# Performance work log

Measured on AMD Instinct MI355X. Metric: run time of the kernel, lower is better.

Reference implementation:

```python
import jax, jax.numpy as jnp
import numpy as np

REFN, RN, G = 4, 2, 1          # reference views, query-group repeat, n_groups
NH, DH = 4, 32                 # heads, head channels
C = NH * DH                    # 128
H = W = 64
STRIDE, KS = 2, 3
HK, WK = H // STRIDE, W // STRIDE
L = 2048                       # query tokens per batch element
OFR = 2.0                      # offset_range_factor
SCALE = DH ** -0.5


def _grid_sample(img, grid):
    # img: (N, Ch, H, W); grid: (N, Hg, Wg, 2) xy in [-1,1]
    # bilinear, align_corners=True, padding_mode='zeros' (matches F.grid_sample)
    N, Ch, Hh, Ww = img.shape
    gx = (grid[..., 0] + 1.0) * 0.5 * (Ww - 1)
    gy = (grid[..., 1] + 1.0) * 0.5 * (Hh - 1)
    x0 = jnp.floor(gx); y0 = jnp.floor(gy)
    x1, y1 = x0 + 1.0, y0 + 1.0

    def gather(xi, yi):
        valid = ((xi >= 0) & (xi <= Ww - 1) & (yi >= 0) & (yi <= Hh - 1))
        xc = jnp.clip(xi, 0, Ww - 1).astype(jnp.int32)
        yc = jnp.clip(yi, 0, Hh - 1).astype(jnp.int32)
        g = jax.vmap(lambda im, yy, xx: im[:, yy, xx])(img, yc, xc)  # (N,Ch,Hg,Wg)
        return g * valid[:, None].astype(img.dtype)

    wa = (x1 - gx) * (y1 - gy); wb = (gx - x0) * (y1 - gy)
    wc = (x1 - gx) * (gy - y0); wd = (gx - x0) * (gy - y0)
    return (gather(x0, y0) * wa[:, None] + gather(x1, y0) * wb[:, None]
            + gather(x0, y1) * wc[:, None] + gather(x1, y1) * wd[:, None])


def setup_inputs():
    key = jax.random.key(0)
    ks = jax.random.split(key, 10)
    s = 0.05  # keep logits in a sane range with random weights
    return {
        "x": jax.random.normal(ks[0], (REFN, C, H, W), jnp.float32),
        "y": jax.random.normal(ks[1], (REFN, C, H, W), jnp.float32),
        "q_": jax.random.normal(ks[2], (RN * REFN, L, C), jnp.float32),
        "mask_": jnp.ones((RN * REFN, L, 1), jnp.float32),
        "Wq": jax.random.normal(ks[3], (C, C), jnp.float32) * s,
        "bq": jnp.zeros((C,), jnp.float32),
        "Wmd": jax.random.normal(ks[4], (C, C), jnp.float32) * s,
        "dw_w": jax.random.normal(ks[5], (C, 1, KS, KS), jnp.float32) * s,
        "dw_b": jnp.zeros((C,), jnp.float32),
        "ln_g": jnp.ones((C,), jnp.float32),
        "ln_b": jnp.zeros((C,), jnp.float32),
        "off_w": jax.random.normal(ks[6], (2, C), jnp.float32) * s,
        "Wk": jax.random.normal(ks[7], (C, C), jnp.float32) * s,
        "bk": jnp.zeros((C,), jnp.float32),
        "Wv": jax.random.normal(ks[8], (C, C), jnp.float32) * s,
        "bv": jnp.zeros((C,), jnp.float32),
        "Wo": jax.random.normal(ks[9], (C, C), jnp.float32) * s,
        "bo": jnp.zeros((C,), jnp.float32),
    }


def _forward(x, y, q_, mask_, Wq, bq, Wmd, dw_w, dw_b, ln_g, ln_b, off_w,
             Wk, bk, Wv, bv, Wo, bo):
    B = q_.shape[0]
    # masked mean over tokens -> modulation vector, then proj_q (Linear)
    q_cond = jnp.sum(q_ * mask_, 1) / (jnp.sum(mask_, 1) + 1e-6)   # (B, C)
    q_cond = q_cond @ Wq.T + bq

    xb = jnp.tile(x, (RN, 1, 1, 1))                                 # (B, C, H, W)

    # Conv2DMod (StyleGAN2 modulated 1x1 conv, demod eps 1e-8)
    wmod = Wmd[None] * (q_cond[:, None, :] + 1.0)                   # (B, Cout, Cin)
    wmod = wmod * jax.lax.rsqrt(jnp.sum(wmod * wmod, -1, keepdims=True) + 1e-8)
    q_t = jnp.einsum('boi,bihw->bohw', wmod, xb)                    # (B, C, H, W)

    # conv_offset: depthwise 3x3 s2 -> LayerNorm(channel) -> GELU -> 1x1 (no bias)
    t = jax.lax.conv_general_dilated(
        q_t, dw_w, (STRIDE, STRIDE), ((1, 1), (1, 1)),
        feature_group_count=C, dimension_numbers=('NCHW', 'OIHW', 'NCHW'))
    t = t + dw_b[None, :, None, None]
    mu = jnp.mean(t, 1, keepdims=True)
    var = jnp.mean((t - mu) ** 2, 1, keepdims=True)
    t = (t - mu) * jax.lax.rsqrt(var + 1e-5)
    t = t * ln_g[None, :, None, None] + ln_b[None, :, None, None]
    t = jax.nn.gelu(t, approximate=False)
    offset = jnp.einsum('oc,bchw->bohw', off_w, t)                  # (B*G, 2, HK, WK)

    orange = jnp.array([1.0 / (HK - 1), 1.0 / (WK - 1)], jnp.float32).reshape(1, 2, 1, 1)
    offset = jnp.tanh(offset) * orange * OFR
    offset = jnp.transpose(offset, (0, 2, 3, 1))                    # (B*G, HK, WK, 2) yx

    ry = (jnp.linspace(0.5, HK - 0.5, HK) / (HK - 1.0)) * 2.0 - 1.0
    rx = (jnp.linspace(0.5, WK - 0.5, WK) / (WK - 1.0)) * 2.0 - 1.0
    ref = jnp.stack(jnp.meshgrid(ry, rx, indexing='ij'), -1)        # (HK, WK, 2) yx
    ref = jnp.broadcast_to(ref[None], (B * G, HK, WK, 2))

    pos = offset + ref            # offset_range_factor >= 0 -> no clamp
    pos = pos[..., ::-1]          # yx -> xy for grid_sample
    ns = HK * WK
    # '(rn refn gn) h w n -> (refn gn) rn (h w) n'  (G == 1)
    grid = pos.reshape(RN, REFN, ns, 2).transpose(1, 0, 2, 3)       # (REFN, RN, ns, 2)

    xs = _grid_sample(y, grid)                                      # (REFN, C, RN, ns)
    # 'refn c (rn gn) (h w) -> (rn refn gn) c h w'  (G == 1)
    xs = xs.transpose(2, 0, 1, 3).reshape(B, C, ns)                 # (B, C, ns)

    k = (jnp.einsum('oc,bcn->bon', Wk, xs) + bk[None, :, None]).reshape(B * NH, DH, ns)
    v = (jnp.einsum('oc,bcn->bon', Wv, xs) + bv[None, :, None]).reshape(B * NH, DH, ns)
    q = jnp.transpose(q_, (0, 2, 1)).reshape(B * NH, DH, -1)        # (B*NH, DH, L)

    attn = jnp.einsum('bcm,bcn->bmn', q, k) * SCALE                 # (B*NH, L, ns)
    # NOTE: original calls attn.masked_fill(...) WITHOUT assignment (non in-place)
    # so the mask has no effect on attention -- faithfully omitted.
    attn = jax.nn.softmax(attn, axis=-1)
    out = jnp.einsum('bmn,bcn->bcm', attn, v)                       # (B*NH, DH, L)
    out = out.reshape(B, C, -1).transpose(0, 2, 1)                  # (B, L, C), G == 1
    yo = out @ Wo.T + bo
    return yo, grid.reshape(B, G, HK, WK, 2), ref.reshape(B, G, HK, WK, 2)


def reference(x, y, q_, mask_, Wq, bq, Wmd, dw_w, dw_b, ln_g, ln_b, off_w,
              Wk, bk, Wv, bv, Wo, bo):
    return _forward(x, y, q_, mask_, Wq, bq, Wmd, dw_w, dw_b, ln_g, ln_b, off_w,
                    Wk, bk, Wv, bv, Wo, bo)
```

## Files before the change

### kernel.cpp

```cpp
#include <hip/hip_runtime.h>
#include <math.h>


#define SCALE_F 0.17677669529663687f

typedef __attribute__((ext_vector_type(8))) short short8v;
typedef __attribute__((ext_vector_type(8))) unsigned short u16x8;
typedef __attribute__((ext_vector_type(4))) unsigned short u16x4;
typedef __attribute__((ext_vector_type(4))) float f32x4;

static __device__ __forceinline__ unsigned short f2bf(float f) {
  unsigned int u = __builtin_bit_cast(unsigned int, f);
  u += 0x7fffu + ((u >> 16) & 1u);
  return (unsigned short)(u >> 16);
}

__global__ void kt_wb(const float* __restrict__ Wk, const float* __restrict__ Wv,
                      const float* __restrict__ Wo, unsigned short* __restrict__ Wkb,
                      unsigned short* __restrict__ Wvb, unsigned short* __restrict__ Wob) {
  int idx = blockIdx.x * 256 + threadIdx.x;
  Wkb[idx] = f2bf(Wk[idx]);
  Wvb[idx] = f2bf(Wv[idx]);
  Wob[idx] = f2bf(Wo[idx]);
}

__global__ void kt_transpose_y(const float* __restrict__ y, float* __restrict__ y_t) {
  __shared__ __align__(16) float tile[128][65];
  int bid = blockIdx.x;
  int n = bid >> 6, yy = bid & 63;
  int t = threadIdx.x;
  for (int p = 0; p < 32; ++p) {
    int idx = p * 256 + t;
    int c = idx >> 6, xx = idx & 63;
    tile[c][xx] = y[((n * 128 + c) * 64 + yy) * 64 + xx];
  }
  __syncthreads();
  for (int p = 0; p < 32; ++p) {
    int idx = p * 256 + t;
    int xx = idx >> 7, c = idx & 127;
    y_t[((n * 64 + yy) * 64 + xx) * 128 + c] = tile[c][xx];
  }
}

__global__ void kt_xT(const float* __restrict__ x, unsigned short* __restrict__ xTb) {
  __shared__ float tile[128][65];
  int bid = blockIdx.x;
  int n = bid >> 6, yy = bid & 63;
  int t = threadIdx.x;
  for (int p = 0; p < 32; ++p) {
    int idx = p * 256 + t;
    int c = idx >> 6, xx = idx & 63;
    tile[c][xx] = x[((n * 128 + c) * 64 + yy) * 64 + xx];
  }
  __syncthreads();
  for (int p = 0; p < 4; ++p) {
    int idx = p * 256 + t;
    int xx = idx >> 4, g = idx & 15;
    u16x8 v;
#pragma unroll
    for (int j = 0; j < 8; ++j) v[j] = f2bf(tile[g * 8 + j][xx]);
    *reinterpret_cast<u16x8*>(
        xTb + ((size_t)n * 4096 + yy * 64 + xx) * 128 + g * 8) = v;
  }
}

__global__ void k_qsum(const float* __restrict__ q_, const float* __restrict__ mask_,
                       float* __restrict__ qpart, float* __restrict__ mpart) {
  int b = blockIdx.x, ch = blockIdx.y, c = threadIdx.x;
  float acc = 0.f, ma = 0.f;
  for (int mm = 0; mm < 64; ++mm) {
    int m = ch * 64 + mm;
    float mk = mask_[b * 2048 + m];
    acc += q_[(b * 2048 + m) * 128 + c] * mk;
    ma += mk;
  }
  qpart[(b * 32 + ch) * 128 + c] = acc;
  if (c == 0) mpart[b * 32 + ch] = ma;
}

__global__ void k_wmod(const float* __restrict__ qpart, const float* __restrict__ mpart,
                       const float* __restrict__ Wq, const float* __restrict__ bq,
                       const float* __restrict__ Wmd, unsigned short* __restrict__ wmodb) {
  int b = blockIdx.x, c = threadIdx.x;
  __shared__ float qc[128], q2[128];
  float s = 0.f, ms = 0.f;
  for (int ch = 0; ch < 32; ++ch) {
    s += qpart[(b * 32 + ch) * 128 + c];
    ms += mpart[b * 32 + ch];
  }
  qc[c] = s / (ms + 1e-6f);
  __syncthreads();
  float acc = bq[c];
  for (int i = 0; i < 128; ++i) acc += qc[i] * Wq[c * 128 + i];
  q2[c] = acc + 1.0f;
  __syncthreads();
  float nrm = 0.f;
  for (int i = 0; i < 128; ++i) {
    float wv = Wmd[c * 128 + i] * q2[i];
    nrm += wv * wv;
  }
  float rs = 1.0f / sqrtf(nrm + 1e-8f);
  for (int i = 0; i < 128; ++i)
    wmodb[(b * 128 + c) * 128 + i] = f2bf(Wmd[c * 128 + i] * q2[i] * rs);
}

__global__ __launch_bounds__(256) void k_qt_mfma(
    const unsigned short* __restrict__ wmodb,
    const unsigned short* __restrict__ xTb,
    float* __restrict__ q_t) {
  int b = blockIdx.x;
  int n0 = blockIdx.y * 128;
  int t = threadIdx.x;
  int w = t >> 6, l = t & 63;
  int lr = l & 15, lg = l >> 4;

  __shared__ __align__(16) unsigned short Asw[128 * 128];
  __shared__ __align__(16) unsigned short Bsw[128 * 128];
  char* Ab = reinterpret_cast<char*>(Asw);
  char* Bb = reinterpret_cast<char*>(Bsw);

  const unsigned short* asrc = wmodb + (size_t)b * 128 * 128;
  const unsigned short* bsrc = xTb + ((size_t)(b & 3) * 4096 + n0) * 128;
#pragma unroll
  for (int it = 0; it < 8; ++it) {
    int idx = it * 256 + t;
    int row = idx >> 4, cb = (idx & 15) * 16;
    int dst = row * 256 + (cb ^ ((row & 7) << 4));
    *reinterpret_cast<u16x8*>(Ab + dst) = *reinterpret_cast<const u16x8*>(asrc + idx * 8);
    *reinterpret_cast<u16x8*>(Bb + dst) = *reinterpret_cast<const u16x8*>(bsrc + idx * 8);
  }
  __syncthreads();

  const f32x4 z4 = {0.f, 0.f, 0.f, 0.f};
  f32x4 acc[8][2];
#pragma unroll
  for (int mf = 0; mf < 8; ++mf) { acc[mf][0] = z4; acc[mf][1] = z4; }

#pragma unroll
  for (int ks = 0; ks < 4; ++ks) {
    int cb = ks * 64 + lg * 16;
    short8v bf[2];
#pragma unroll
    for (int nf = 0; nf < 2; ++nf) {
      int row = w * 32 + nf * 16 + lr;
      bf[nf] = *reinterpret_cast<const short8v*>(Bb + row * 256 + (cb ^ ((row & 7) << 4)));
    }
#pragma unroll
    for (int mf = 0; mf < 8; ++mf) {
      int row = mf * 16 + lr;
      short8v af = *reinterpret_cast<const short8v*>(Ab + row * 256 + (cb ^ ((row & 7) << 4)));
      acc[mf][0] = __builtin_amdgcn_mfma_f32_16x16x32_bf16(af, bf[0], acc[mf][0], 0, 0, 0);
      acc[mf][1] = __builtin_amdgcn_mfma_f32_16x16x32_bf16(af, bf[1], acc[mf][1], 0, 0, 0);
    }
  }

#pragma unroll
  for (int mf = 0; mf < 8; ++mf)
#pragma unroll
    for (int nf = 0; nf < 2; ++nf)
#pragma unroll
      for (int r = 0; r < 4; ++r) {
        int o = mf * 16 + lg * 4 + r;
        int px = n0 + w * 32 + nf * 16 + lr;
        q_t[((size_t)(b * 128 + o)) * 4096 + px] = acc[mf][nf][r];
      }
}

__global__ void k_dwconv(const float* __restrict__ q_t, const float* __restrict__ dw_w,
                         const float* __restrict__ dw_b, float* __restrict__ t0) {
  int bid = blockIdx.x;
  int t = threadIdx.x;
  int b = bid >> 9;
  int c = (bid >> 2) & 127;
  int px = (bid & 3) * 256 + t;
  int i = px >> 5, j = px & 31;
  float w[9];
#pragma unroll
  for (int q = 0; q < 9; ++q) w[q] = dw_w[c * 9 + q];
  const float* src = q_t + (b * 128 + c) * 4096;
  float acc = dw_b[c];
#pragma unroll
  for (int dy = 0; dy < 3; ++dy) {
    int yy = 2 * i - 1 + dy;
    if (yy < 0 || yy > 63) continue;
#pragma unroll
    for (int dx = 0; dx < 3; ++dx) {
      int xx = 2 * j - 1 + dx;
      if (xx < 0 || xx > 63) continue;
      acc += w[dy * 3 + dx] * src[yy * 64 + xx];
    }
  }
  t0[(b * 128 + c) * 1024 + px] = acc;
}

__global__ void k_ln_off(const float* __restrict__ t0, const float* __restrict__ ln_g,
                         const float* __restrict__ ln_b, const float* __restrict__ off_w,
                         float* __restrict__ posg, float* __restrict__ grid_out,
                         float* __restrict__ ref_out) {
  int b = blockIdx.x;
  int s = blockIdx.y * 64 + threadIdx.x;
  int i = s >> 5, j = s & 31;
  const float* src = t0 + b * 128 * 1024 + s;
  float sum = 0.f, sq = 0.f;
  for (int c = 0; c < 128; ++c) {
    float v = src[c * 1024];
    sum += v; sq += v * v;
  }
  float mu = sum * (1.0f / 128.0f);
  float var = sq * (1.0f / 128.0f) - mu * mu;
  float rstd = 1.0f / sqrtf(var + 1e-5f);
  float off0 = 0.f, off1 = 0.f;
  for (int c = 0; c < 128; ++c) {
    float v = src[c * 1024];
    float xn = (v - mu) * rstd * ln_g[c] + ln_b[c];
    float g = 0.5f * xn * (1.0f + erff(xn * 0.7071067811865476f));
    off0 += off_w[c] * g;
    off1 += off_w[128 + c] * g;
  }
  float offy = tanhf(off0) * (1.0f / 31.0f) * 2.0f;
  float offx = tanhf(off1) * (1.0f / 31.0f) * 2.0f;
  float ry = (0.5f + (float)i) / 31.0f * 2.0f - 1.0f;
  float rx = (0.5f + (float)j) / 31.0f * 2.0f - 1.0f;
  float posy = offy + ry;
  float posx = offx + rx;
  int bp = (b & 3) * 2 + (b >> 2);
  float2 g2; g2.x = posx; g2.y = posy;
  *reinterpret_cast<float2*>(&grid_out[(bp * 1024 + s) * 2]) = g2;
  float2 r2; r2.x = ry; r2.y = rx;
  *reinterpret_cast<float2*>(&ref_out[(b * 1024 + s) * 2]) = r2;
  float2 p2;
  p2.x = (posx + 1.0f) * 0.5f * 63.0f;
  p2.y = (posy + 1.0f) * 0.5f * 63.0f;
  *reinterpret_cast<float2*>(&posg[(b * 1024 + s) * 2]) = p2;
}

__global__ void k_gsample(const float* __restrict__ y_t, const float* __restrict__ posg,
                          unsigned short* __restrict__ xsb) {
  int b = blockIdx.x;
  int s = blockIdx.y * 2 + (threadIdx.x >> 7);
  int c = threadIdx.x & 127;
  float gx = posg[(b * 1024 + s) * 2 + 0];
  float gy = posg[(b * 1024 + s) * 2 + 1];
  float x0 = floorf(gx), y0 = floorf(gy);
  float x1 = x0 + 1.0f, y1 = y0 + 1.0f;
  float wa = (x1 - gx) * (y1 - gy);
  float wb = (gx - x0) * (y1 - gy);
  float wc = (x1 - gx) * (gy - y0);
  float wd = (gx - x0) * (gy - y0);
  int n = b & 3;
  const float* base = y_t + n * 64 * 64 * 128 + c;
  float acc = 0.f;
  if (x0 >= 0.f && x0 <= 63.f && y0 >= 0.f && y0 <= 63.f)
    acc += wa * base[((int)y0 * 64 + (int)x0) * 128];
  if (x1 >= 0.f && x1 <= 63.f && y0 >= 0.f && y0 <= 63.f)
    acc += wb * base[((int)y0 * 64 + (int)x1) * 128];
  if (x0 >= 0.f && x0 <= 63.f && y1 >= 0.f && y1 <= 63.f)
    acc += wc * base[((int)y1 * 64 + (int)x0) * 128];
  if (x1 >= 0.f && x1 <= 63.f && y1 >= 0.f && y1 <= 63.f)
    acc += wd * base[((int)y1 * 64 + (int)x1) * 128];
  xsb[(b * 1024 + s) * 128 + c] = f2bf(acc);
}

__global__ __launch_bounds__(256) void k_projkv_mfma(
    const unsigned short* __restrict__ xsb, const unsigned short* __restrict__ Wkb,
    const unsigned short* __restrict__ Wvb, const float* __restrict__ bk,
    const float* __restrict__ bv, unsigned short* __restrict__ kb,
    unsigned short* __restrict__ vb) {
  int b = blockIdx.x, nt = blockIdx.y, z = blockIdx.z;
  int t = threadIdx.x;
  int w = t >> 6, l = t & 63;
  int lr = l & 15, lg = l >> 4;

  __shared__ __align__(16) unsigned short Asw[128 * 128];
  __shared__ __align__(16) unsigned short Bsw[128 * 128];
  char* Ab = reinterpret_cast<char*>(Asw);
  char* Bb = reinterpret_cast<char*>(Bsw);

  const unsigned short* asrc = (z == 0) ? Wkb : Wvb;
  const unsigned short* bsrc = xsb + ((size_t)b * 1024 + nt * 128) * 128;
  const float* bias = (z == 0) ? bk : bv;
#pragma unroll
  for (int it = 0; it < 8; ++it) {
    int idx = it * 256 + t;
    int row = idx >> 4, cb = (idx & 15) * 16;
    int dst = row * 256 + (cb ^ ((row & 7) << 4));
    *reinterpret_cast<u16x8*>(Ab + dst) = *reinterpret_cast<const u16x8*>(asrc + idx * 8);
    *reinterpret_cast<u16x8*>(Bb + dst) = *reinterpret_cast<const u16x8*>(bsrc + idx * 8);
  }
  __syncthreads();

  const f32x4 z4 = {0.f, 0.f, 0.f, 0.f};
  f32x4 acc[8][2];
#pragma unroll
  for (int mf = 0; mf < 8; ++mf) { acc[mf][0] = z4; acc[mf][1] = z4; }

#pragma unroll
  for (int ks = 0; ks < 4; ++ks) {
    int cb = ks * 64 + lg * 16;
    short8v bf[2];
#pragma unroll
    for (int nf = 0; nf < 2; ++nf) {
      int row = w * 32 + nf * 16 + lr;
      bf[nf] = *reinterpret_cast<const short8v*>(Bb + row * 256 + (cb ^ ((row & 7) << 4)));
    }
#pragma unroll
    for (int mf = 0; mf < 8; ++mf) {
      int row = mf * 16 + lr;
      short8v af = *reinterpret_cast<const short8v*>(Ab + row * 256 + (cb ^ ((row & 7) << 4)));
      acc[mf][0] = __builtin_amdgcn_mfma_f32_16x16x32_bf16(af, bf[0], acc[mf][0], 0, 0, 0);
      acc[mf][1] = __builtin_amdgcn_mfma_f32_16x16x32_bf16(af, bf[1], acc[mf][1], 0, 0, 0);
    }
  }

  if (z == 0) {
#pragma unroll
    for (int mf = 0; mf < 8; ++mf) {
      int o0 = mf * 16 + lg * 4;
      int h = o0 >> 5, d0 = o0 & 31;
#pragma unroll
      for (int nf = 0; nf < 2; ++nf) {
        int n = nt * 128 + w * 32 + nf * 16 + lr;
        u16x4 pk;
#pragma unroll
        for (int r = 0; r < 4; ++r) pk[r] = f2bf(acc[mf][nf][r] + bias[o0 + r]);
        *reinterpret_cast<u16x4*>(kb + ((size_t)(b * 4 + h) * 1024 + n) * 32 + d0) = pk;
      }
    }
  } else {
#pragma unroll
    for (int mf = 0; mf < 8; ++mf)
#pragma unroll
      for (int nf = 0; nf < 2; ++nf)
#pragma unroll
        for (int r = 0; r < 4; ++r) {
          int o = mf * 16 + lg * 4 + r;
          int n = nt * 128 + w * 32 + nf * 16 + lr;
          vb[(size_t)(b * 128 + o) * 1024 + n] = f2bf(acc[mf][nf][r] + bias[o]);
        }
  }
}

__global__ __launch_bounds__(256) void k_attn_mfma(
    const float* __restrict__ q_, const unsigned short* __restrict__ kb,
    const unsigned short* __restrict__ vb, unsigned short* __restrict__ obmcb) {
  int bh = blockIdx.x;
  int b = bh >> 2, h = bh & 3;
  int m0 = blockIdx.y * 128;
  int t = threadIdx.x;
  int w = t >> 6, l = t & 63;
  int lr = l & 15, lg = l >> 4;

  __shared__ __align__(16) unsigned short K_lds[4 * 64 * 8];
  __shared__ __align__(16) unsigned short V_lds[8 * 32 * 8];
  __shared__ __align__(16) unsigned short P_lds[4 * 256 * 8];

  short8v qa[2];
#pragma unroll
  for (int mf = 0; mf < 2; ++mf) {
    int m = m0 + w * 32 + mf * 16 + lr;
    const float* qp = q_ + ((size_t)(b * 2048 + m)) * 128 + h * 32 + lg * 8;
    float4 x0 = *reinterpret_cast<const float4*>(qp);
    float4 x1 = *reinterpret_cast<const float4*>(qp + 4);
    float vals[8] = {x0.x, x0.y, x0.z, x0.w, x1.x, x1.y, x1.z, x1.w};
    short8v q8;
#pragma unroll
    for (int j = 0; j < 8; ++j) q8[j] = (short)f2bf(vals[j] * SCALE_F);
    qa[mf] = q8;
  }

  const f32x4 z4 = {0.f, 0.f, 0.f, 0.f};
  f32x4 oacc[2][2];
  float lsum[2][4];
#pragma unroll
  for (int mf = 0; mf < 2; ++mf) {
#pragma unroll
    for (int df = 0; df < 2; ++df) oacc[mf][df] = z4;
#pragma unroll
    for (int r = 0; r < 4; ++r) lsum[mf][r] = 0.f;
  }

  const unsigned short* kbase = kb + (size_t)bh * 1024 * 32;
  const unsigned short* vbase = vb + (size_t)bh * 32 * 1024;

  for (int nt = 0; nt < 16; ++nt) {
    __syncthreads();
    {
      int dblk = t >> 6, n = t & 63;
      u16x8 kv = *reinterpret_cast<const u16x8*>(kbase + ((size_t)(nt * 64 + n)) * 32 + dblk * 8);
      *reinterpret_cast<u16x8*>(&K_lds[t * 8]) = kv;
    }
    {
      int nblk = t >> 5, d = t & 31;
      u16x8 vv = *reinterpret_cast<const u16x8*>(vbase + (size_t)d * 1024 + nt * 64 + nblk * 8);
      *reinterpret_cast<u16x8*>(&V_lds[t * 8]) = vv;
    }
    __syncthreads();

    short8v kfr[4];
#pragma unroll
    for (int nf = 0; nf < 4; ++nf)
      kfr[nf] = *reinterpret_cast<const short8v*>(&K_lds[(lg * 64 + nf * 16 + lr) * 8]);
    f32x4 s[2][4];
#pragma unroll
    for (int mf = 0; mf < 2; ++mf)
#pragma unroll
      for (int nf = 0; nf < 4; ++nf)
        s[mf][nf] = __builtin_amdgcn_mfma_f32_16x16x32_bf16(qa[mf], kfr[nf], z4, 0, 0, 0);

#pragma unroll
    for (int mf = 0; mf < 2; ++mf) {
#pragma unroll
      for (int nf = 0; nf < 4; ++nf) {
        int sbase = (w * 256 + (nf * 2 + (lr >> 3)) * 32 + mf * 16 + lg * 4) * 8 + (lr & 7);
#pragma unroll
        for (int r = 0; r < 4; ++r) {
          float pe = __expf(s[mf][nf][r]);
          lsum[mf][r] += pe;
          P_lds[sbase + r * 8] = f2bf(pe);
        }
      }
    }
    __syncthreads();

#pragma unroll
    for (int ks = 0; ks < 2; ++ks) {
      short8v pa[2], vf[2];
#pragma unroll
      for (int mf = 0; mf < 2; ++mf)
        pa[mf] = *reinterpret_cast<const short8v*>(
            &P_lds[(w * 256 + (ks * 4 + lg) * 32 + mf * 16 + lr) * 8]);
#pragma unroll
      for (int df = 0; df < 2; ++df)
        vf[df] = *reinterpret_cast<const short8v*>(
            &V_lds[((ks * 4 + lg) * 32 + df * 16 + lr) * 8]);
#pragma unroll
      for (int mf = 0; mf < 2; ++mf)
#pragma unroll
        for (int df = 0; df < 2; ++df)
          oacc[mf][df] = __builtin_amdgcn_mfma_f32_16x16x32_bf16(pa[mf], vf[df], oacc[mf][df], 0, 0, 0);
    }
  }

#pragma unroll
  for (int mf = 0; mf < 2; ++mf) {
#pragma unroll
    for (int r = 0; r < 4; ++r) {
      float v = lsum[mf][r];
      v += __shfl_xor(v, 1); v += __shfl_xor(v, 2);
      v += __shfl_xor(v, 4); v += __shfl_xor(v, 8);
      float inv = 1.0f / v;
      int m = m0 + w * 32 + mf * 16 + lg * 4 + r;
      unsigned short* op = obmcb + ((size_t)(b * 2048 + m)) * 128 + h * 32;
      op[lr] = f2bf(oacc[mf][0][r] * inv);
      op[16 + lr] = f2bf(oacc[mf][1][r] * inv);
    }
  }
}

__global__ __launch_bounds__(256) void k_out_mfma(
    const unsigned short* __restrict__ obmcb, const unsigned short* __restrict__ Wob,
    const float* __restrict__ bo, float* __restrict__ yo) {
  int b = blockIdx.x, mt = blockIdx.y;
  int t = threadIdx.x;
  int w = t >> 6, l = t & 63;
  int lr = l & 15, lg = l >> 4;

  __shared__ __align__(16) unsigned short Asw[128 * 128];
  __shared__ __align__(16) unsigned short Bsw[128 * 128];
  char* Ab = reinterpret_cast<char*>(Asw);
  char* Bb = reinterpret_cast<char*>(Bsw);

  const unsigned short* bsrc = obmcb + ((size_t)b * 2048 + mt * 128) * 128;
#pragma unroll
  for (int it = 0; it < 8; ++it) {
    int idx = it * 256 + t;
    int row = idx >> 4, cb = (idx & 15) * 16;
    int dst = row * 256 + (cb ^ ((row & 7) << 4));
    *reinterpret_cast<u16x8*>(Ab + dst) = *reinterpret_cast<const u16x8*>(Wob + idx * 8);
    *reinterpret_cast<u16x8*>(Bb + dst) = *reinterpret_cast<const u16x8*>(bsrc + idx * 8);
  }
  __syncthreads();

  const f32x4 z4 = {0.f, 0.f, 0.f, 0.f};
  f32x4 acc[8][2];
#pragma unroll
  for (int mf = 0; mf < 8; ++mf) { acc[mf][0] = z4; acc[mf][1] = z4; }

#pragma unroll
  for (int ks = 0; ks < 4; ++ks) {
    int cb = ks * 64 + lg * 16;
    short8v bf[2];
#pragma unroll
    for (int nf = 0; nf < 2; ++nf) {
      int row = w * 32 + nf * 16 + lr;
      bf[nf] = *reinterpret_cast<const short8v*>(Bb + row * 256 + (cb ^ ((row & 7) << 4)));
    }
#pragma unroll
    for (int mf = 0; mf < 8; ++mf) {
      int row = mf * 16 + lr;
      short8v af = *reinterpret_cast<const short8v*>(Ab + row * 256 + (cb ^ ((row & 7) << 4)));
      acc[mf][0] = __builtin_amdgcn_mfma_f32_16x16x32_bf16(af, bf[0], acc[mf][0], 0, 0, 0);
      acc[mf][1] = __builtin_amdgcn_mfma_f32_16x16x32_bf16(af, bf[1], acc[mf][1], 0, 0, 0);
    }
  }

#pragma unroll
  for (int mf = 0; mf < 8; ++mf) {
    int o0 = mf * 16 + lg * 4;
#pragma unroll
    for (int nf = 0; nf < 2; ++nf) {
      int m = mt * 128 + w * 32 + nf * 16 + lr;
      float4 rv;
      rv.x = acc[mf][nf][0] + bo[o0 + 0];
      rv.y = acc[mf][nf][1] + bo[o0 + 1];
      rv.z = acc[mf][nf][2] + bo[o0 + 2];
      rv.w = acc[mf][nf][3] + bo[o0 + 3];
      *reinterpret_cast<float4*>(&yo[((size_t)(b * 2048 + m)) * 128 + o0]) = rv;
    }
  }
}

extern "C" void kernel_launch(void* const* d_in, const int* in_sizes, int n_in,
                              void* d_out, int out_size, void* d_ws, size_t ws_size,
                              hipStream_t stream) {
  const float* x     = (const float*)d_in[0];
  const float* y     = (const float*)d_in[1];
  const float* q_    = (const float*)d_in[2];
  const float* mask_ = (const float*)d_in[3];
  const float* Wq    = (const float*)d_in[4];
  const float* bq    = (const float*)d_in[5];
  const float* Wmd   = (const float*)d_in[6];
  const float* dw_w  = (const float*)d_in[7];
  const float* dw_b  = (const float*)d_in[8];
  const float* ln_g  = (const float*)d_in[9];
  const float* ln_b  = (const float*)d_in[10];
  const float* off_w = (const float*)d_in[11];
  const float* Wk    = (const float*)d_in[12];
  const float* bk    = (const float*)d_in[13];
  const float* Wv    = (const float*)d_in[14];
  const float* bv    = (const float*)d_in[15];
  const float* Wo    = (const float*)d_in[16];
  const float* bo    = (const float*)d_in[17];

  float* out = (float*)d_out;
  float* yo       = out;
  float* grid_out = out + 2097152;
  float* ref_out  = grid_out + 16384;

  float* ws    = (float*)d_ws;
  float* y_t   = ws;
  float* qpart = y_t + 2097152;
  float* mpart = qpart + 32768;
  float* q_t   = mpart + 256;
  float* t0    = q_t + 4194304;
  float* posg  = t0 + 1048576;
  unsigned short* kbb   = (unsigned short*)(posg + 16384);
  unsigned short* vbb   = kbb + 1048576;
  unsigned short* xTb   = vbb + 1048576;
  unsigned short* wmodb = xTb + 2097152;
  unsigned short* xsb   = wmodb + 131072;
  unsigned short* obmcb = xsb + 1048576;
  unsigned short* Wkb   = obmcb + 2097152;
  unsigned short* Wvb   = Wkb + 16384;
  unsigned short* Wob   = Wvb + 16384;

  hipLaunchKernelGGL(kt_wb, dim3(64), dim3(256), 0, stream, Wk, Wv, Wo, Wkb, Wvb, Wob);
  hipLaunchKernelGGL(kt_transpose_y, dim3(256), dim3(256), 0, stream, y, y_t);
  hipLaunchKernelGGL(kt_xT, dim3(256), dim3(256), 0, stream, x, xTb);
  hipLaunchKernelGGL(k_qsum, dim3(8, 32), dim3(128), 0, stream, q_, mask_, qpart, mpart);
  hipLaunchKernelGGL(k_wmod, dim3(8), dim3(128), 0, stream,
                     qpart, mpart, Wq, bq, Wmd, wmodb);
  hipLaunchKernelGGL(k_qt_mfma, dim3(8, 32), dim3(256), 0, stream, wmodb, xTb, q_t);
  hipLaunchKernelGGL(k_dwconv, dim3(4096), dim3(256), 0, stream, q_t, dw_w, dw_b, t0);
  hipLaunchKernelGGL(k_ln_off, dim3(8, 16), dim3(64), 0, stream,
                     t0, ln_g, ln_b, off_w, posg, grid_out, ref_out);
  hipLaunchKernelGGL(k_gsample, dim3(8, 512), dim3(256), 0, stream, y_t, posg, xsb);
  hipLaunchKernelGGL(k_projkv_mfma, dim3(8, 8, 2), dim3(256), 0, stream,
                     xsb, Wkb, Wvb, bk, bv, kbb, vbb);
  hipLaunchKernelGGL(k_attn_mfma, dim3(32, 16), dim3(256), 0, stream, q_, kbb, vbb, obmcb);
  hipLaunchKernelGGL(k_out_mfma, dim3(8, 16), dim3(256), 0, stream, obmcb, Wob, bo, yo);
}
```

Before: 215.8 us.

## Merge pack kernels, bf16 q_t, parallel LN reduce, double-buffer attention K/V

Merges the y and x transpose kernels into one launch and drops the weight-conversion kernel by converting Wk/Wv/Wo to bf16 while loading tiles in the consuming GEMMs. Stores the modulated query map in bf16 to halve the traffic into the depthwise conv. Gives the LayerNorm/offset kernel 256 threads with a shared tile and cross-group reduction. Double-buffers K/V in the attention loop with register prefetch, and swizzles the P tile to cut bank conflicts and barriers. The bf16 intermediate adds rounding error to the offsets and sampling positions.

```diff
diff --git a/kernel.cpp b/kernel.cpp
--- a/kernel.cpp
+++ b/kernel.cpp
@@ -14,53 +14,47 @@
   u += 0x7fffu + ((u >> 16) & 1u);
   return (unsigned short)(u >> 16);
 }
-
-__global__ void kt_wb(const float* __restrict__ Wk, const float* __restrict__ Wv,
-                      const float* __restrict__ Wo, unsigned short* __restrict__ Wkb,
-                      unsigned short* __restrict__ Wvb, unsigned short* __restrict__ Wob) {
-  int idx = blockIdx.x * 256 + threadIdx.x;
-  Wkb[idx] = f2bf(Wk[idx]);
-  Wvb[idx] = f2bf(Wv[idx]);
-  Wob[idx] = f2bf(Wo[idx]);
-}
-
-__global__ void kt_transpose_y(const float* __restrict__ y, float* __restrict__ y_t) {
+static __device__ __forceinline__ float bf2f(unsigned short s) {
+  unsigned int u = ((unsigned int)s) << 16;
+  return __builtin_bit_cast(float, u);
+}
+
+__global__ void kt_pack(const float* __restrict__ y, const float* __restrict__ x,
+                        float* __restrict__ y_t, unsigned short* __restrict__ xTb) {
   __shared__ __align__(16) float tile[128][65];
   int bid = blockIdx.x;
-  int n = bid >> 6, yy = bid & 63;
   int t = threadIdx.x;
-  for (int p = 0; p < 32; ++p) {
-    int idx = p * 256 + t;
-    int c = idx >> 6, xx = idx & 63;
-    tile[c][xx] = y[((n * 128 + c) * 64 + yy) * 64 + xx];
-  }
-  __syncthreads();
-  for (int p = 0; p < 32; ++p) {
-    int idx = p * 256 + t;
-    int xx = idx >> 7, c = idx & 127;
-    y_t[((n * 64 + yy) * 64 + xx) * 128 + c] = tile[c][xx];
-  }
-}
-
-__global__ void kt_xT(const float* __restrict__ x, unsigned short* __restrict__ xTb) {
-  __shared__ float tile[128][65];
-  int bid = blockIdx.x;
-  int n = bid >> 6, yy = bid & 63;
-  int t = threadIdx.x;
-  for (int p = 0; p < 32; ++p) {
-    int idx = p * 256 + t;
-    int c = idx >> 6, xx = idx & 63;
-    tile[c][xx] = x[((n * 128 + c) * 64 + yy) * 64 + xx];
-  }
-  __syncthreads();
-  for (int p = 0; p < 4; ++p) {
-    int idx = p * 256 + t;
-    int xx = idx >> 4, g = idx & 15;
-    u16x8 v;
-#pragma unroll
-    for (int j = 0; j < 8; ++j) v[j] = f2bf(tile[g * 8 + j][xx]);
-    *reinterpret_cast<u16x8*>(
-        xTb + ((size_t)n * 4096 + yy * 64 + xx) * 128 + g * 8) = v;
+  if (bid < 256) {
+    int n = bid >> 6, yy = bid & 63;
+    for (int p = 0; p < 32; ++p) {
+      int idx = p * 256 + t;
+      int c = idx >> 6, xx = idx & 63;
+      tile[c][xx] = y[((n * 128 + c) * 64 + yy) * 64 + xx];
+    }
+    __syncthreads();
+    for (int p = 0; p < 32; ++p) {
+      int idx = p * 256 + t;
+      int xx = idx >> 7, c = idx & 127;
+      y_t[((n * 64 + yy) * 64 + xx) * 128 + c] = tile[c][xx];
+    }
+  } else {
+    int nb = bid - 256;
+    int n = nb >> 6, yy = nb & 63;
+    for (int p = 0; p < 32; ++p) {
+      int idx = p * 256 + t;
+      int c = idx >> 6, xx = idx & 63;
+      tile[c][xx] = x[((n * 128 + c) * 64 + yy) * 64 + xx];
+    }
+    __syncthreads();
+    for (int p = 0; p < 4; ++p) {
+      int idx = p * 256 + t;
+      int xx = idx >> 4, g = idx & 15;
+      u16x8 v;
+#pragma unroll
+      for (int j = 0; j < 8; ++j) v[j] = f2bf(tile[g * 8 + j][xx]);
+      *reinterpret_cast<u16x8*>(
+          xTb + ((size_t)n * 4096 + yy * 64 + xx) * 128 + g * 8) = v;
+    }
   }
 }
 
@@ -107,7 +101,7 @@
 __global__ __launch_bounds__(256) void k_qt_mfma(
     const unsigned short* __restrict__ wmodb,
     const unsigned short* __restrict__ xTb,
-    float* __restrict__ q_t) {
+    unsigned short* __restrict__ q_tb) {
   int b = blockIdx.x;
   int n0 = blockIdx.y * 128;
   int t = threadIdx.x;
@@ -162,11 +156,12 @@
       for (int r = 0; r < 4; ++r) {
         int o = mf * 16 + lg * 4 + r;
         int px = n0 + w * 32 + nf * 16 + lr;
-        q_t[((size_t)(b * 128 + o)) * 4096 + px] = acc[mf][nf][r];
+        q_tb[((size_t)(b * 128 + o)) * 4096 + px] = f2bf(acc[mf][nf][r]);
       }
 }
 
-__global__ void k_dwconv(const float* __restrict__ q_t, const float* __restrict__ dw_w,
+__global__ void k_dwconv(const unsigned short* __restrict__ q_tb,
+                         const float* __restrict__ dw_w,
                          const float* __restrict__ dw_b, float* __restrict__ t0) {
   int bid = blockIdx.x;
   int t = threadIdx.x;
@@ -177,7 +172,7 @@
   float w[9];
 #pragma unroll
   for (int q = 0; q < 9; ++q) w[q] = dw_w[c * 9 + q];
-  const float* src = q_t + (b * 128 + c) * 4096;
+  const unsigned short* src = q_tb + (size_t)(b * 128 + c) * 4096;
   float acc = dw_b[c];
 #pragma unroll
   for (int dy = 0; dy < 3; ++dy) {
@@ -187,51 +182,76 @@
     for (int dx = 0; dx < 3; ++dx) {
       int xx = 2 * j - 1 + dx;
       if (xx < 0 || xx > 63) continue;
-      acc += w[dy * 3 + dx] * src[yy * 64 + xx];
+      acc += w[dy * 3 + dx] * bf2f(src[yy * 64 + xx]);
     }
   }
   t0[(b * 128 + c) * 1024 + px] = acc;
 }
 
-__global__ void k_ln_off(const float* __restrict__ t0, const float* __restrict__ ln_g,
-                         const float* __restrict__ ln_b, const float* __restrict__ off_w,
-                         float* __restrict__ posg, float* __restrict__ grid_out,
-                         float* __restrict__ ref_out) {
+__global__ __launch_bounds__(256) void k_ln_off(
+    const float* __restrict__ t0, const float* __restrict__ ln_g,
+    const float* __restrict__ ln_b, const float* __restrict__ off_w,
+    float* __restrict__ posg, float* __restrict__ grid_out,
+    float* __restrict__ ref_out) {
   int b = blockIdx.x;
-  int s = blockIdx.y * 64 + threadIdx.x;
-  int i = s >> 5, j = s & 31;
-  const float* src = t0 + b * 128 * 1024 + s;
+  int s0 = blockIdx.y * 64;
+  int t = threadIdx.x;
+  __shared__ float tile[128][64];
+  __shared__ float red0[4][64], red1[4][64];
+
+  for (int p = 0; p < 32; ++p) {
+    int idx = p * 256 + t;
+    int c = idx >> 6, s = idx & 63;
+    tile[c][s] = t0[(b * 128 + c) * 1024 + s0 + s];
+  }
+  __syncthreads();
+
+  int s = t & 63, cg = t >> 6;
   float sum = 0.f, sq = 0.f;
-  for (int c = 0; c < 128; ++c) {
-    float v = src[c * 1024];
+  for (int cc = 0; cc < 32; ++cc) {
+    float v = tile[cg * 32 + cc][s];
     sum += v; sq += v * v;
   }
-  float mu = sum * (1.0f / 128.0f);
-  float var = sq * (1.0f / 128.0f) - mu * mu;
+  red0[cg][s] = sum; red1[cg][s] = sq;
+  __syncthreads();
+  float tsum = red0[0][s] + red0[1][s] + red0[2][s] + red0[3][s];
+  float tsq  = red1[0][s] + red1[1][s] + red1[2][s] + red1[3][s];
+  float mu = tsum * (1.0f / 128.0f);
+  float var = tsq * (1.0f / 128.0f) - mu * mu;
   float rstd = 1.0f / sqrtf(var + 1e-5f);
-  float off0 = 0.f, off1 = 0.f;
-  for (int c = 0; c < 128; ++c) {
-    float v = src[c * 1024];
+  float o0 = 0.f, o1 = 0.f;
+  for (int cc = 0; cc < 32; ++cc) {
+    int c = cg * 32 + cc;
+    float v = tile[c][s];
     float xn = (v - mu) * rstd * ln_g[c] + ln_b[c];
     float g = 0.5f * xn * (1.0f + erff(xn * 0.7071067811865476f));
-    off0 += off_w[c] * g;
-    off1 += off_w[128 + c] * g;
-  }
-  float offy = tanhf(off0) * (1.0f / 31.0f) * 2.0f;
-  float offx = tanhf(off1) * (1.0f / 31.0f) * 2.0f;
-  float ry = (0.5f + (float)i) / 31.0f * 2.0f - 1.0f;
-  float rx = (0.5f + (float)j) / 31.0f * 2.0f - 1.0f;
-  float posy = offy + ry;
-  float posx = offx + rx;
-  int bp = (b & 3) * 2 + (b >> 2);
-  float2 g2; g2.x = posx; g2.y = posy;
-  *reinterpret_cast<float2*>(&grid_out[(bp * 1024 + s) * 2]) = g2;
-  float2 r2; r2.x = ry; r2.y = rx;
-  *reinterpret_cast<float2*>(&ref_out[(b * 1024 + s) * 2]) = r2;
-  float2 p2;
-  p2.x = (posx + 1.0f) * 0.5f * 63.0f;
-  p2.y = (posy + 1.0f) * 0.5f * 63.0f;
-  *reinterpret_cast<float2*>(&posg[(b * 1024 + s) * 2]) = p2;
+    o0 += off_w[c] * g;
+    o1 += off_w[128 + c] * g;
+  }
+  __syncthreads();
+  red0[cg][s] = o0; red1[cg][s] = o1;
+  __syncthreads();
+  if (t < 64) {
+    float off0 = red0[0][s] + red0[1][s] + red0[2][s] + red0[3][s];
+    float off1 = red1[0][s] + red1[1][s] + red1[2][s] + red1[3][s];
+    float offy = tanhf(off0) * (1.0f / 31.0f) * 2.0f;
+    float offx = tanhf(off1) * (1.0f / 31.0f) * 2.0f;
+    int sg = s0 + s;
+    int i = sg >> 5, j = sg & 31;
+    float ry = (0.5f + (float)i) / 31.0f * 2.0f - 1.0f;
+    float rx = (0.5f + (float)j) / 31.0f * 2.0f - 1.0f;
+    float posy = offy + ry;
+    float posx = offx + rx;
+    int bp = (b & 3) * 2 + (b >> 2);
+    float2 g2; g2.x = posx; g2.y = posy;
+    *reinterpret_cast<float2*>(&grid_out[(bp * 1024 + sg) * 2]) = g2;
+    float2 r2; r2.x = ry; r2.y = rx;
+    *reinterpret_cast<float2*>(&ref_out[(b * 1024 + sg) * 2]) = r2;
+    float2 p2;
+    p2.x = (posx + 1.0f) * 0.5f * 63.0f;
+    p2.y = (posy + 1.0f) * 0.5f * 63.0f;
+    *reinterpret_cast<float2*>(&posg[(b * 1024 + sg) * 2]) = p2;
+  }
 }
 
 __global__ void k_gsample(const float* __restrict__ y_t, const float* __restrict__ posg,
@@ -262,8 +282,8 @@
 }
 
 __global__ __launch_bounds__(256) void k_projkv_mfma(
-    const unsigned short* __restrict__ xsb, const unsigned short* __restrict__ Wkb,
-    const unsigned short* __restrict__ Wvb, const float* __restrict__ bk,
+    const unsigned short* __restrict__ xsb, const float* __restrict__ Wk,
+    const float* __restrict__ Wv, const float* __restrict__ bk,
     const float* __restrict__ bv, unsigned short* __restrict__ kb,
     unsigned short* __restrict__ vb) {
   int b = blockIdx.x, nt = blockIdx.y, z = blockIdx.z;
@@ -276,7 +296,7 @@
   char* Ab = reinterpret_cast<char*>(Asw);
   char* Bb = reinterpret_cast<char*>(Bsw);
 
-  const unsigned short* asrc = (z == 0) ? Wkb : Wvb;
+  const float* asrcf = (z == 0) ? Wk : Wv;
   const unsigned short* bsrc = xsb + ((size_t)b * 1024 + nt * 128) * 128;
   const float* bias = (z == 0) ? bk : bv;
 #pragma unroll
@@ -284,7 +304,12 @@
     int idx = it * 256 + t;
     int row = idx >> 4, cb = (idx & 15) * 16;
     int dst = row * 256 + (cb ^ ((row & 7) << 4));
-    *reinterpret_cast<u16x8*>(Ab + dst) = *reinterpret_cast<const u16x8*>(asrc + idx * 8);
+    float4 f0 = *reinterpret_cast<const float4*>(asrcf + idx * 8);
+    float4 f1 = *reinterpret_cast<const float4*>(asrcf + idx * 8 + 4);
+    u16x8 av;
+    av[0] = f2bf(f0.x); av[1] = f2bf(f0.y); av[2] = f2bf(f0.z); av[3] = f2bf(f0.w);
+    av[4] = f2bf(f1.x); av[5] = f2bf(f1.y); av[6] = f2bf(f1.z); av[7] = f2bf(f1.w);
+    *reinterpret_cast<u16x8*>(Ab + dst) = av;
     *reinterpret_cast<u16x8*>(Bb + dst) = *reinterpret_cast<const u16x8*>(bsrc + idx * 8);
   }
   __syncthreads();
@@ -350,9 +375,9 @@
   int w = t >> 6, l = t & 63;
   int lr = l & 15, lg = l >> 4;
 
-  __shared__ __align__(16) unsigned short K_lds[4 * 64 * 8];
-  __shared__ __align__(16) unsigned short V_lds[8 * 32 * 8];
-  __shared__ __align__(16) unsigned short P_lds[4 * 256 * 8];
+  __shared__ __align__(16) unsigned short K_lds[2][2048];
+  __shared__ __align__(16) unsigned short V_lds[2][2048];
+  __shared__ __align__(16) unsigned short P_lds[8192];
 
   short8v qa[2];
 #pragma unroll
@@ -368,6 +393,17 @@
     qa[mf] = q8;
   }
 
+  const unsigned short* kbase = kb + (size_t)bh * 1024 * 32;
+  const unsigned short* vbase = vb + (size_t)bh * 32 * 1024;
+  int ksl_n = t & 63, ksl_d = t >> 6;
+  int vsl_d = t & 31, vsl_nb = t >> 5;
+
+  u16x8 kreg = *reinterpret_cast<const u16x8*>(kbase + ((size_t)ksl_n) * 32 + ksl_d * 8);
+  u16x8 vreg = *reinterpret_cast<const u16x8*>(vbase + (size_t)vsl_d * 1024 + vsl_nb * 8);
+  *reinterpret_cast<u16x8*>(&K_lds[0][t * 8]) = kreg;
+  *reinterpret_cast<u16x8*>(&V_lds[0][t * 8]) = vreg;
+  __syncthreads();
+
   const f32x4 z4 = {0.f, 0.f, 0.f, 0.f};
   f32x4 oacc[2][2];
   float lsum[2][4];
@@ -379,27 +415,21 @@
     for (int r = 0; r < 4; ++r) lsum[mf][r] = 0.f;
   }
 
-  const unsigned short* kbase = kb + (size_t)bh * 1024 * 32;
-  const unsigned short* vbase = vb + (size_t)bh * 32 * 1024;
-
+  int swzW = ((lr >> 3) & 1) << 3;
+  int swzR = (lg & 1) << 3;
+  int cur = 0;
   for (int nt = 0; nt < 16; ++nt) {
-    __syncthreads();
-    {
-      int dblk = t >> 6, n = t & 63;
-      u16x8 kv = *reinterpret_cast<const u16x8*>(kbase + ((size_t)(nt * 64 + n)) * 32 + dblk * 8);
-      *reinterpret_cast<u16x8*>(&K_lds[t * 8]) = kv;
-    }
-    {
-      int nblk = t >> 5, d = t & 31;
-      u16x8 vv = *reinterpret_cast<const u16x8*>(vbase + (size_t)d * 1024 + nt * 64 + nblk * 8);
-      *reinterpret_cast<u16x8*>(&V_lds[t * 8]) = vv;
-    }
-    __syncthreads();
+    if (nt < 15) {
+      kreg = *reinterpret_cast<const u16x8*>(
+          kbase + ((size_t)((nt + 1) * 64 + ksl_n)) * 32 + ksl_d * 8);
+      vreg = *reinterpret_cast<const u16x8*>(
+          vbase + (size_t)vsl_d * 1024 + (nt + 1) * 64 + vsl_nb * 8);
+    }
 
     short8v kfr[4];
 #pragma unroll
     for (int nf = 0; nf < 4; ++nf)
-      kfr[nf] = *reinterpret_cast<const short8v*>(&K_lds[(lg * 64 + nf * 16 + lr) * 8]);
+      kfr[nf] = *reinterpret_cast<const short8v*>(&K_lds[cur][(lg * 64 + nf * 16 + lr) * 8]);
     f32x4 s[2][4];
 #pragma unroll
     for (int mf = 0; mf < 2; ++mf)
@@ -416,11 +446,10 @@
         for (int r = 0; r < 4; ++r) {
           float pe = __expf(s[mf][nf][r]);
           lsum[mf][r] += pe;
-          P_lds[sbase + r * 8] = f2bf(pe);
+          P_lds[(sbase + r * 8) ^ swzW] = f2bf(pe);
         }
       }
     }
-    __syncthreads();
 
 #pragma unroll
     for (int ks = 0; ks < 2; ++ks) {
@@ -428,16 +457,23 @@
 #pragma unroll
       for (int mf = 0; mf < 2; ++mf)
         pa[mf] = *reinterpret_cast<const short8v*>(
-            &P_lds[(w * 256 + (ks * 4 + lg) * 32 + mf * 16 + lr) * 8]);
+            &P_lds[((w * 256 + (ks * 4 + lg) * 32 + mf * 16 + lr) * 8) ^ swzR]);
 #pragma unroll
       for (int df = 0; df < 2; ++df)
         vf[df] = *reinterpret_cast<const short8v*>(
-            &V_lds[((ks * 4 + lg) * 32 + df * 16 + lr) * 8]);
+            &V_lds[cur][((ks * 4 + lg) * 32 + df * 16 + lr) * 8]);
 #pragma unroll
       for (int mf = 0; mf < 2; ++mf)
 #pragma unroll
         for (int df = 0; df < 2; ++df)
           oacc[mf][df] = __builtin_amdgcn_mfma_f32_16x16x32_bf16(pa[mf], vf[df], oacc[mf][df], 0, 0, 0);
+    }
+
+    if (nt < 15) {
+      *reinterpret_cast<u16x8*>(&K_lds[cur ^ 1][t * 8]) = kreg;
+      *reinterpret_cast<u16x8*>(&V_lds[cur ^ 1][t * 8]) = vreg;
+      __syncthreads();
+      cur ^= 1;
     }
   }
 
@@ -458,7 +494,7 @@
 }
 
 __global__ __launch_bounds__(256) void k_out_mfma(
-    const unsigned short* __restrict__ obmcb, const unsigned short* __restrict__ Wob,
+    const unsigned short* __restrict__ obmcb, const float* __restrict__ Wo,
     const float* __restrict__ bo, float* __restrict__ yo) {
   int b = blockIdx.x, mt = blockIdx.y;
   int t = threadIdx.x;
@@ -476,7 +512,12 @@
     int idx = it * 256 + t;
     int row = idx >> 4, cb = (idx & 15) * 16;
     int dst = row * 256 + (cb ^ ((row & 7) << 4));
-    *reinterpret_cast<u16x8*>(Ab + dst) = *reinterpret_cast<const u16x8*>(Wob + idx * 8);
+    float4 f0 = *reinterpret_cast<const float4*>(Wo + idx * 8);
+    float4 f1 = *reinterpret_cast<const float4*>(Wo + idx * 8 + 4);
+    u16x8 av;
+    av[0] = f2bf(f0.x); av[1] = f2bf(f0.y); av[2] = f2bf(f0.z); av[3] = f2bf(f0.w);
+    av[4] = f2bf(f1.x); av[5] = f2bf(f1.y); av[6] = f2bf(f1.z); av[7] = f2bf(f1.w);
+    *reinterpret_cast<u16x8*>(Ab + dst) = av;
     *reinterpret_cast<u16x8*>(Bb + dst) = *reinterpret_cast<const u16x8*>(bsrc + idx * 8);
   }
   __syncthreads();
@@ -551,8 +592,7 @@
   float* y_t   = ws;
   float* qpart = y_t + 2097152;
   float* mpart = qpart + 32768;
-  float* q_t   = mpart + 256;
-  float* t0    = q_t + 4194304;
+  float* t0    = mpart + 256;
   float* posg  = t0 + 1048576;
   unsigned short* kbb   = (unsigned short*)(posg + 16384);
   unsigned short* vbb   = kbb + 1048576;
@@ -560,23 +600,19 @@
   unsigned short* wmodb = xTb + 2097152;
   unsigned short* xsb   = wmodb + 131072;
   unsigned short* obmcb = xsb + 1048576;
-  unsigned short* Wkb   = obmcb + 2097152;
-  unsigned short* Wvb   = Wkb + 16384;
-  unsigned short* Wob   = Wvb + 16384;
-
-  hipLaunchKernelGGL(kt_wb, dim3(64), dim3(256), 0, stream, Wk, Wv, Wo, Wkb, Wvb, Wob);
-  hipLaunchKernelGGL(kt_transpose_y, dim3(256), dim3(256), 0, stream, y, y_t);
-  hipLaunchKernelGGL(kt_xT, dim3(256), dim3(256), 0, stream, x, xTb);
+  unsigned short* q_tb  = obmcb + 2097152;
+
+  hipLaunchKernelGGL(kt_pack, dim3(512), dim3(256), 0, stream, y, x, y_t, xTb);
   hipLaunchKernelGGL(k_qsum, dim3(8, 32), dim3(128), 0, stream, q_, mask_, qpart, mpart);
   hipLaunchKernelGGL(k_wmod, dim3(8), dim3(128), 0, stream,
                      qpart, mpart, Wq, bq, Wmd, wmodb);
-  hipLaunchKernelGGL(k_qt_mfma, dim3(8, 32), dim3(256), 0, stream, wmodb, xTb, q_t);
-  hipLaunchKernelGGL(k_dwconv, dim3(4096), dim3(256), 0, stream, q_t, dw_w, dw_b, t0);
-  hipLaunchKernelGGL(k_ln_off, dim3(8, 16), dim3(64), 0, stream,
+  hipLaunchKernelGGL(k_qt_mfma, dim3(8, 32), dim3(256), 0, stream, wmodb, xTb, q_tb);
+  hipLaunchKernelGGL(k_dwconv, dim3(4096), dim3(256), 0, stream, q_tb, dw_w, dw_b, t0);
+  hipLaunchKernelGGL(k_ln_off, dim3(8, 16), dim3(256), 0, stream,
                      t0, ln_g, ln_b, off_w, posg, grid_out, ref_out);
   hipLaunchKernelGGL(k_gsample, dim3(8, 512), dim3(256), 0, stream, y_t, posg, xsb);
   hipLaunchKernelGGL(k_projkv_mfma, dim3(8, 8, 2), dim3(256), 0, stream,
-                     xsb, Wkb, Wvb, bk, bv, kbb, vbb);
+                     xsb, Wk, Wv, bk, bv, kbb, vbb);
   hipLaunchKernelGGL(k_attn_mfma, dim3(32, 16), dim3(256), 0, stream, q_, kbb, vbb, obmcb);
-  hipLaunchKernelGGL(k_out_mfma, dim3(8, 16), dim3(256), 0, stream, obmcb, Wob, bo, yo);
-}
+  hipLaunchKernelGGL(k_out_mfma, dim3(8, 16), dim3(256), 0, stream, obmcb, Wo, bo, yo);
+}
```

Result: faster. 183.5 us (-15.0%).
